# Kernel optimization log

Hardware: AMD Instinct MI355X
Metric: run time of the kernel (lower is better)

## Reference

```python
import jax, jax.numpy as jnp
import numpy as np

N_NODES = 50000
N_EDGES = 800000
F_IN = 128
HID = 32
H_IN = 4
N_CLS = 47
H_OUT = 4
NEG_SLOPE = 0.2


def _param(k, shape, scale=0.1):
    return jax.random.normal(k, shape, dtype=jnp.float32) * scale


def setup_inputs() -> dict:
    key = jax.random.key(0)
    ks = jax.random.split(key, 14)
    return {
        "x": jax.random.normal(ks[0], (N_NODES, F_IN), dtype=jnp.float32),
        "edge_index": jax.random.randint(ks[1], (2, N_EDGES), 0, N_NODES, dtype=jnp.int64),
        # layer 1: in -> hidden, heads_in, concat
        "W1": _param(ks[2], (F_IN, H_IN * HID)),
        "a1s": _param(ks[3], (H_IN, HID)),
        "a1d": _param(ks[4], (H_IN, HID)),
        "b1": _param(ks[5], (H_IN * HID,)),
        # layer 2: hidden*heads -> hidden, heads_in, concat
        "W2": _param(ks[6], (H_IN * HID, H_IN * HID)),
        "a2s": _param(ks[7], (H_IN, HID)),
        "a2d": _param(ks[8], (H_IN, HID)),
        "b2": _param(ks[9], (H_IN * HID,)),
        # layer 3: hidden*heads -> out, heads_out, mean (concat=False)
        "W3": _param(ks[10], (H_IN * HID, H_OUT * N_CLS)),
        "a3s": _param(ks[11], (H_OUT, N_CLS)),
        "a3d": _param(ks[12], (H_OUT, N_CLS)),
        "b3": _param(ks[13], (N_CLS,)),
    }


def gat_conv(x, W, att_src, att_dst, bias, src, dst, concat):
    """PyG GATConv (self-loops pre-appended in src/dst, eval mode)."""
    n = x.shape[0]
    H, C = att_src.shape
    h = (x @ W).reshape(n, H, C)                      # [N, H, C]
    a_src = jnp.sum(h * att_src[None], axis=-1)       # [N, H]
    a_dst = jnp.sum(h * att_dst[None], axis=-1)       # [N, H]
    alpha = a_src[src] + a_dst[dst]                   # [E, H]
    alpha = jnp.where(alpha >= 0, alpha, NEG_SLOPE * alpha)
    # segment softmax over destination nodes
    m = jax.ops.segment_max(alpha, dst, num_segments=n)  # [N, H]
    e = jnp.exp(alpha - m[dst])
    denom = jax.ops.segment_sum(e, dst, num_segments=n)  # [N, H]
    w = e / denom[dst]                                   # [E, H]
    msg = h[src] * w[:, :, None]                         # [E, H, C]
    out = jax.ops.segment_sum(msg, dst, num_segments=n)  # [N, H, C]
    if concat:
        out = out.reshape(n, H * C)
    else:
        out = out.mean(axis=1)
    return out + bias


def reference(x, edge_index, W1, a1s, a1d, b1, W2, a2s, a2d, b2, W3, a3s, a3d, b3):
    n = x.shape[0]
    loops = jnp.arange(n, dtype=edge_index.dtype)
    src = jnp.concatenate([edge_index[0], loops])
    dst = jnp.concatenate([edge_index[1], loops])
    h = gat_conv(x, W1, a1s, a1d, b1, src, dst, concat=True)
    h = jax.nn.relu(h)
    h = gat_conv(h, W2, a2s, a2d, b2, src, dst, concat=True)
    h = jax.nn.relu(h)
    h = gat_conv(h, W3, a3s, a3d, b3, src, dst, concat=False)
    return jax.nn.log_softmax(h, axis=1)
```

## Files before the change

### kernel.cpp

```cpp
#include <hip/hip_runtime.h>

typedef unsigned short u16;
typedef unsigned int uint32;
typedef __attribute__((ext_vector_type(8))) short short8;
typedef __attribute__((ext_vector_type(4))) float float4v;

#define N_NODES 50000
#define N_EDGES 800000
#define N_TOT   850000
#define NBH 256
#define NB_BKT ((N_NODES + 255) >> 8)
#define NODE_BLOCKS ((N_NODES + 3) / 4)

__device__ __forceinline__ float b2f(u16 u) {
  return __uint_as_float(((unsigned int)u) << 16);
}
__device__ __forceinline__ u16 f2b(float f) {
  unsigned int x = __float_as_uint(f);
  unsigned int r = (x + 0x7fffu + ((x >> 16) & 1u)) >> 16;
  return (u16)r;
}
__device__ __forceinline__ float lo_bf(uint32 g) { return __uint_as_float(g << 16); }
__device__ __forceinline__ float hi_bf(uint32 g) { return __uint_as_float(g & 0xffff0000u); }
__device__ __forceinline__ u16 conv_elem(const void* src, int i, int isf32) {
  if (isf32) return f2b(((const float*)src)[i]);
  return ((const u16*)src)[i];
}
__device__ __forceinline__ float lrelu(float a) { return (a >= 0.f) ? a : 0.2f * a; }
__device__ __forceinline__ int eget(const int* __restrict__ ei, int i, int isI64) {
  return isI64 ? ei[2 * i] : ei[i];
}

__global__ void detect_mode(const u16* __restrict__ x16, const int* __restrict__ ei32,
                            int* __restrict__ flags) {
  __shared__ int sh_f32, sh_i32;
  int tid = threadIdx.x;
  if (tid == 0) { sh_f32 = 0; sh_i32 = 0; }
  __syncthreads();
  int emax = 0;
  for (int i = tid; i < 4096; i += 256) {
    int e = (x16[i] >> 7) & 0xFF;
    emax = emax > e ? emax : e;
  }
  if (emax >= 140) atomicOr(&sh_f32, 1);
  if (ei32[2 * tid + 1] != 0) atomicOr(&sh_i32, 1);
  __syncthreads();
  if (tid == 0) { flags[0] = sh_f32; flags[1] = sh_i32 ? 0 : 1; }
}

__global__ void reorder_all(const void* W1, const void* W2, const void* W3,
                            const void* a1s, const void* a1d, const void* b1,
                            const void* a2s, const void* a2d, const void* b2,
                            const void* a3s, const void* a3d, const void* b3,
                            const int* __restrict__ flags,
                            u16* __restrict__ Wf1, u16* __restrict__ Wf2,
                            u16* __restrict__ Wf3, u16* __restrict__ wt) {
  int idx = blockIdx.x * blockDim.x + threadIdx.x;
  int f32 = flags[0];
  if (idx < 57344) {
    const void* W; u16* Wf; int NCOLS, li;
    if (idx < 16384)      { W = W1; Wf = Wf1; NCOLS = 128; li = idx; }
    else if (idx < 32768) { W = W2; Wf = Wf2; NCOLS = 128; li = idx - 16384; }
    else                  { W = W3; Wf = Wf3; NCOLS = 188; li = idx - 32768; }
    int j = li & 7;
    int l = (li >> 3) & 63;
    int c = (li >> 9) & 3;
    int t = li >> 11;
    int k = c * 32 + (l >> 4) * 8 + j;
    int n = t * 16 + (l & 15);
    Wf[li] = (n < NCOLS) ? conv_elem(W, k * NCOLS + n, f32) : (u16)0;
  } else {
    int li = idx - 57344;
    const void* src; int off;
    if (li < 128)       { src = a1s; off = 16384; }
    else if (li < 256)  { src = a1d; off = 16512; li -= 128; }
    else if (li < 384)  { src = b1;  off = 16640; li -= 256; }
    else if (li < 512)  { src = a2s; off = 33152; li -= 384; }
    else if (li < 640)  { src = a2d; off = 33280; li -= 512; }
    else if (li < 768)  { src = b2;  off = 33408; li -= 640; }
    else if (li < 956)  { src = a3s; off = 57600; li -= 768; }
    else if (li < 1144) { src = a3d; off = 57788; li -= 956; }
    else if (li < 1191) { src = b3;  off = 57976; li -= 1144; }
    else return;
    wt[off + li] = conv_elem(src, li, f32);
  }
}


__global__ __launch_bounds__(256) void pack_hist(const int* __restrict__ ei,
                                                 const int* __restrict__ flags,
                                                 uint32* __restrict__ epack,
                                                 int* __restrict__ cnt, int nE) {
  __shared__ int hist[NB_BKT];
  for (int t = threadIdx.x; t < NB_BKT; t += 256) hist[t] = 0;
  __syncthreads();
  const int i64 = flags[1];
  const int chunk = (nE + NBH - 1) / NBH;
  const int lo = blockIdx.x * chunk;
  const int hi = min(lo + chunk, nE);
  for (int e = lo + (int)threadIdx.x; e < hi; e += 256) {
    int s = eget(ei, e, i64);
    int d = eget(ei, nE + e, i64);
    epack[e] = ((uint32)d << 16) | (uint32)s;
    atomicAdd(&hist[d >> 8], 1);
  }
  __syncthreads();
  for (int t = threadIdx.x; t < NB_BKT; t += 256) cnt[t * NBH + blockIdx.x] = hist[t];
}

__global__ __launch_bounds__(256) void scan_cols(int* __restrict__ cnt,
                                                 int* __restrict__ total) {
  __shared__ int ws[4];
  const int bkt = blockIdx.x;
  const int tid = threadIdx.x, lane = tid & 63, wv = tid >> 6;
  int v = cnt[bkt * NBH + tid];
  int incl = v;
#pragma unroll
  for (int off = 1; off < 64; off <<= 1) {
    int t = __shfl_up(incl, off, 64);
    if (lane >= off) incl += t;
  }
  if (lane == 63) ws[wv] = incl;
  __syncthreads();
  if (tid == 0) {
    int s = 0;
#pragma unroll
    for (int w = 0; w < 4; w++) { int t = ws[w]; ws[w] = s; s += t; }
    total[bkt] = s;
  }
  __syncthreads();
  cnt[bkt * NBH + tid] = ws[wv] + incl - v;
}

__global__ __launch_bounds__(256) void scan_base(const int* __restrict__ total,
                                                 int* __restrict__ base) {
  __shared__ int ws[4];
  const int tid = threadIdx.x, lane = tid & 63, wv = tid >> 6;
  int v = (tid < NB_BKT) ? total[tid] : 0;
  int incl = v;
#pragma unroll
  for (int off = 1; off < 64; off <<= 1) {
    int t = __shfl_up(incl, off, 64);
    if (lane >= off) incl += t;
  }
  if (lane == 63) ws[wv] = incl;
  __syncthreads();
  if (tid == 0) {
    int s = 0;
#pragma unroll
    for (int w = 0; w < 4; w++) { int t = ws[w]; ws[w] = s; s += t; }
    base[NB_BKT] = s;
  }
  __syncthreads();
  if (tid < NB_BKT) base[tid] = ws[wv] + incl - v;
}

__global__ __launch_bounds__(256) void scatter_coarse(const uint32* __restrict__ epack,
                                                      const int* __restrict__ cnt,
                                                      const int* __restrict__ base,
                                                      uint32* __restrict__ staging, int nE) {
  __shared__ int lcur[NB_BKT];
  for (int t = threadIdx.x; t < NB_BKT; t += 256)
    lcur[t] = base[t] + cnt[t * NBH + blockIdx.x];
  __syncthreads();
  const int chunk = (nE + NBH - 1) / NBH;
  const int lo = blockIdx.x * chunk;
  const int hi = min(lo + chunk, nE);
  for (int e = lo + (int)threadIdx.x; e < hi; e += 256) {
    uint32 pk = epack[e];
    int p = atomicAdd(&lcur[pk >> 24], 1);
    staging[p] = pk;
  }
}

__global__ __launch_bounds__(256) void build_csr(const uint32* __restrict__ staging,
                                                 const int* __restrict__ base,
                                                 int* __restrict__ row_start,
                                                 u16* __restrict__ csr_dst,
                                                 int* __restrict__ csr_src32, int nN) {
  __shared__ int hist[256];
  __shared__ int cur[256];
  __shared__ int ws[4];
  const int b = blockIdx.x;
  const int tid = threadIdx.x;
  const int lane = tid & 63, wv = tid >> 6;
  hist[tid] = 0;
  __syncthreads();
  const int lo = base[b], hi = base[b + 1];
  for (int i = lo + tid; i < hi; i += 256)
    atomicAdd(&hist[(staging[i] >> 16) & 255], 1);
  __syncthreads();
  int v = hist[tid];
  int incl = v;
#pragma unroll
  for (int off = 1; off < 64; off <<= 1) {
    int t = __shfl_up(incl, off, 64);
    if (lane >= off) incl += t;
  }
  if (lane == 63) ws[wv] = incl;
  __syncthreads();
  if (tid == 0) {
    int s = 0;
#pragma unroll
    for (int w = 0; w < 4; w++) { int t = ws[w]; ws[w] = s; s += t; }
  }
  __syncthreads();
  int excl = ws[wv] + incl - v;
  const int n = (b << 8) + tid;
  if (n < nN) {
    int rs = lo + (b << 8) + excl + tid;
    row_start[n] = rs;
    csr_src32[rs] = n;
    u16 g16 = (u16)n;
    for (int k = 0; k <= v; k++) csr_dst[rs + k] = g16;
    cur[tid] = rs + 1;
  }
  if (b == NB_BKT - 1 && tid == 0) row_start[nN] = N_TOT;
  __syncthreads();
  for (int i = lo + tid; i < hi; i += 256) {
    uint32 pk = staging[i];
    int p = atomicAdd(&cur[(pk >> 16) & 255], 1);
    csr_src32[p] = (int)(pk & 0xffffu);
  }
}

template <int NT, int NCOLS, int STRIDE, bool FUSE_A, bool CMAJOR, bool FUSE3, bool RAWX>
__global__ __launch_bounds__(256) void gemm_mfma(const void* __restrict__ X,
                                                 const u16* __restrict__ Wf,
                                                 const u16* __restrict__ attS,
                                                 const u16* __restrict__ attD,
                                                 const int* __restrict__ flags,
                                                 u16* __restrict__ H,
                                                 float* __restrict__ a_s,
                                                 float* __restrict__ a_d, int M) {
  const int wid = __builtin_amdgcn_readfirstlane(threadIdx.x >> 6);
  const int lane = threadIdx.x & 63;
  const int row0 = (blockIdx.x * 4 + wid) * 16;
  if (row0 >= M) return;
  const int qr = lane >> 4;
  const int ln = lane & 15;

  float4v acc[NT];
#pragma unroll
  for (int t = 0; t < NT; t++) acc[t] = (float4v){0.f, 0.f, 0.f, 0.f};

  const short8* Wf8 = (const short8*)Wf;
  const size_t aoff = (size_t)(row0 + ln) * 128 + qr * 8;
  int f32m = 0;
  if constexpr (RAWX) f32m = flags[0];

#pragma unroll
  for (int c = 0; c < 4; c++) {
    short8 afrag;
    if constexpr (RAWX) {
      if (f32m) {
        const float* ap = (const float*)X + aoff + c * 32;
        float4 lo = ((const float4*)ap)[0];
        float4 hi = ((const float4*)ap)[1];
        afrag[0] = (short)f2b(lo.x); afrag[1] = (short)f2b(lo.y);
        afrag[2] = (short)f2b(lo.z); afrag[3] = (short)f2b(lo.w);
        afrag[4] = (short)f2b(hi.x); afrag[5] = (short)f2b(hi.y);
        afrag[6] = (short)f2b(hi.z); afrag[7] = (short)f2b(hi.w);
      } else {
        afrag = *(const short8*)((const u16*)X + aoff + c * 32);
      }
    } else {
      afrag = *(const short8*)((const u16*)X + aoff + c * 32);
    }
#pragma unroll
    for (int t = 0; t < NT; t++) {
      short8 bfrag = Wf8[(t * 4 + c) * 64 + lane];
      acc[t] = __builtin_amdgcn_mfma_f32_16x16x32_bf16(afrag, bfrag, acc[t], 0, 0, 0);
    }
  }

#pragma unroll
  for (int t = 0; t < NT; t++) {
    int col = t * 16 + ln;
    if (col < NCOLS) {
      int off;
      if constexpr (CMAJOR) {
        int h = (col >= 141) ? 3 : (col >= 94) ? 2 : (col >= 47) ? 1 : 0;
        int c = col - h * 47;
        off = c * 4 + h;
      } else {
        off = col;
      }
#pragma unroll
      for (int i = 0; i < 4; i++) {
        H[(size_t)(row0 + qr * 4 + i) * STRIDE + off] = f2b(acc[t][i]);
      }
    } else {
      if constexpr (CMAJOR) {
#pragma unroll
        for (int i = 0; i < 4; i++) {
          H[(size_t)(row0 + qr * 4 + i) * STRIDE + col] = (u16)0x3F80;
        }
      }
    }
  }

  if constexpr (FUSE_A) {
    float aSf[NT], aDf[NT];
#pragma unroll
    for (int t = 0; t < NT; t++) {
      aSf[t] = b2f(attS[t * 16 + ln]);
      aDf[t] = b2f(attD[t * 16 + ln]);
    }
#pragma unroll
    for (int h = 0; h < 4; h++) {
#pragma unroll
      for (int i = 0; i < 4; i++) {
        float s = acc[2 * h][i] * aSf[2 * h] + acc[2 * h + 1][i] * aSf[2 * h + 1];
        float d = acc[2 * h][i] * aDf[2 * h] + acc[2 * h + 1][i] * aDf[2 * h + 1];
#pragma unroll
        for (int m = 1; m < 16; m <<= 1) {
          s += __shfl_xor(s, m, 64);
          d += __shfl_xor(d, m, 64);
        }
        if (ln == 0) {
          int r = row0 + qr * 4 + i;
          a_s[r * 4 + h] = s;
          a_d[r * 4 + h] = d;
        }
      }
    }
  }

  if constexpr (FUSE3) {
    float sh[4][4], dh[4][4];
#pragma unroll
    for (int h = 0; h < 4; h++)
#pragma unroll
      for (int i = 0; i < 4; i++) { sh[h][i] = 0.f; dh[h][i] = 0.f; }
#pragma unroll
    for (int t = 0; t < NT; t++) {
      int col = t * 16 + ln;
      bool v = (col < NCOLS);
      float aS = v ? b2f(attS[col]) : 0.f;
      float aD = v ? b2f(attD[col]) : 0.f;
      int hh = (col >= 141) ? 3 : (col >= 94) ? 2 : (col >= 47) ? 1 : 0;
      float aS0 = (hh == 0) ? aS : 0.f, aS1 = (hh == 1) ? aS : 0.f;
      float aS2 = (hh == 2) ? aS : 0.f, aS3 = (hh == 3) ? aS : 0.f;
      float aD0 = (hh == 0) ? aD : 0.f, aD1 = (hh == 1) ? aD : 0.f;
      float aD2 = (hh == 2) ? aD : 0.f, aD3 = (hh == 3) ? aD : 0.f;
#pragma unroll
      for (int i = 0; i < 4; i++) {
        float a = acc[t][i];
        sh[0][i] += a * aS0; sh[1][i] += a * aS1;
        sh[2][i] += a * aS2; sh[3][i] += a * aS3;
        dh[0][i] += a * aD0; dh[1][i] += a * aD1;
        dh[2][i] += a * aD2; dh[3][i] += a * aD3;
      }
    }
#pragma unroll
    for (int h = 0; h < 4; h++) {
#pragma unroll
      for (int i = 0; i < 4; i++) {
        float s = sh[h][i], d = dh[h][i];
#pragma unroll
        for (int m = 1; m < 16; m <<= 1) {
          s += __shfl_xor(s, m, 64);
          d += __shfl_xor(d, m, 64);
        }
        if (ln == 0) {
          int r = row0 + qr * 4 + i;
          a_s[r * 4 + h] = s;
          a_d[r * 4 + h] = d;
        }
      }
    }
  }
}

__global__ __launch_bounds__(256) void edge_weights(const int* __restrict__ csr_src,
                                                    const u16* __restrict__ csr_dst,
                                                    const float* __restrict__ a_s,
                                                    const float* __restrict__ a_d,
                                                    uint2* __restrict__ w, int nE) {
  int e = blockIdx.x * blockDim.x + threadIdx.x;
  if (e >= nE) return;
  int s = csr_src[e], d = csr_dst[e];
  float4 as = ((const float4*)a_s)[s];
  float4 ad = ((const float4*)a_d)[d];
  float w0 = __expf(lrelu(as.x + ad.x));
  float w1 = __expf(lrelu(as.y + ad.y));
  float w2 = __expf(lrelu(as.z + ad.z));
  float w3 = __expf(lrelu(as.w + ad.w));
  uint2 o;
  o.x = ((uint32)f2b(w1) << 16) | (uint32)f2b(w0);
  o.y = ((uint32)f2b(w3) << 16) | (uint32)f2b(w2);
  w[e] = o;
}


__global__ __launch_bounds__(256) void aggregate12(const u16* __restrict__ h,
                                                   const float* __restrict__ a_s,
                                                   const float* __restrict__ a_d,
                                                   const int* __restrict__ row_start,
                                                   const int* __restrict__ csr_src,
                                                   const u16* __restrict__ bias,
                                                   u16* __restrict__ out, int nN) {
  const int lane = threadIdx.x & 63;
  const int wid = __builtin_amdgcn_readfirstlane(threadIdx.x >> 6);
  const int n = blockIdx.x * 4 + wid;
  if (n >= nN) return;
  const int hL = lane >> 4;
  const uint32* h32 = (const uint32*)h;
  const float bias0 = b2f(bias[2 * lane]);
  const float bias1 = b2f(bias[2 * lane + 1]);
  const float adv = a_d[n * 4 + hL];
  int beg = row_start[n], end = row_start[n + 1];

  float acc0 = 0.f, acc1 = 0.f, den = 0.f;
  int e = beg;
  for (; e + 3 < end; e += 4) {
    int s[4];
    float av[4];
    uint32 g[4];
#pragma unroll
    for (int j = 0; j < 4; j++) s[j] = csr_src[e + j];
#pragma unroll
    for (int j = 0; j < 4; j++) av[j] = a_s[s[j] * 4 + hL];
#pragma unroll
    for (int j = 0; j < 4; j++) g[j] = h32[s[j] * 64 + lane];
#pragma unroll
    for (int j = 0; j < 4; j++) {
      float w = __expf(lrelu(av[j] + adv));
      den += w;
      acc0 += w * lo_bf(g[j]);
      acc1 += w * hi_bf(g[j]);
    }
  }
  for (; e < end; ++e) {
    int s = csr_src[e];
    float w = __expf(lrelu(a_s[s * 4 + hL] + adv));
    uint32 g = h32[s * 64 + lane];
    den += w;
    acc0 += w * lo_bf(g);
    acc1 += w * hi_bf(g);
  }
  float inv = 1.0f / den;
  float o0 = fmaxf(acc0 * inv + bias0, 0.f);
  float o1 = fmaxf(acc1 * inv + bias1, 0.f);
  uint32 packed = ((uint32)f2b(o1) << 16) | (uint32)f2b(o0);
  ((uint32*)out)[n * 64 + lane] = packed;
}

__global__ __launch_bounds__(256) void aggregate3(const u16* __restrict__ h3,
                                                  const uint2* __restrict__ wbuf,
                                                  const int* __restrict__ row_start,
                                                  const int* __restrict__ csr_src,
                                                  const u16* __restrict__ b3,
                                                  const int* __restrict__ flags,
                                                  void* __restrict__ out, int nN) {
  const int lane = threadIdx.x & 63;
  const int wid = __builtin_amdgcn_readfirstlane(threadIdx.x >> 6);
  const int n = blockIdx.x * 4 + wid;
  if (n >= nN) return;
  const bool act = lane < 47;
  const int lidx = (lane <= 47) ? lane : 0;
  const float b3v = act ? b2f(b3[lane]) : 0.f;
  const int isf32 = flags[0];
  const uint2* h3v = (const uint2*)h3;
  int beg = row_start[n], end = row_start[n + 1];

  float acc0 = 0.f, acc1 = 0.f, acc2 = 0.f, acc3 = 0.f;
  int e = beg;
  for (; e + 7 < end; e += 8) {
    int s[8];
    uint2 wp[8];
    uint2 g[8];
#pragma unroll
    for (int j = 0; j < 8; j++) s[j] = csr_src[e + j];
#pragma unroll
    for (int j = 0; j < 8; j++) wp[j] = wbuf[e + j];
#pragma unroll
    for (int j = 0; j < 8; j++) g[j] = h3v[(size_t)s[j] * 48 + lidx];
#pragma unroll
    for (int j = 0; j < 8; j++) {
      float w0 = lo_bf(wp[j].x), w1 = hi_bf(wp[j].x);
      float w2 = lo_bf(wp[j].y), w3 = hi_bf(wp[j].y);
      acc0 += w0 * lo_bf(g[j].x);
      acc1 += w1 * hi_bf(g[j].x);
      acc2 += w2 * lo_bf(g[j].y);
      acc3 += w3 * hi_bf(g[j].y);
    }
  }
  for (; e + 3 < end; e += 4) {
    int s[4];
    uint2 wp[4];
    uint2 g[4];
#pragma unroll
    for (int j = 0; j < 4; j++) s[j] = csr_src[e + j];
#pragma unroll
    for (int j = 0; j < 4; j++) wp[j] = wbuf[e + j];
#pragma unroll
    for (int j = 0; j < 4; j++) g[j] = h3v[(size_t)s[j] * 48 + lidx];
#pragma unroll
    for (int j = 0; j < 4; j++) {
      float w0 = lo_bf(wp[j].x), w1 = hi_bf(wp[j].x);
      float w2 = lo_bf(wp[j].y), w3 = hi_bf(wp[j].y);
      acc0 += w0 * lo_bf(g[j].x);
      acc1 += w1 * hi_bf(g[j].x);
      acc2 += w2 * lo_bf(g[j].y);
      acc3 += w3 * hi_bf(g[j].y);
    }
  }
  for (; e < end; ++e) {
    int s = csr_src[e];
    uint2 wp = wbuf[e];
    uint2 g = h3v[(size_t)s * 48 + lidx];
    float w0 = lo_bf(wp.x), w1 = hi_bf(wp.x);
    float w2 = lo_bf(wp.y), w3 = hi_bf(wp.y);
    acc0 += w0 * lo_bf(g.x);
    acc1 += w1 * hi_bf(g.x);
    acc2 += w2 * lo_bf(g.y);
    acc3 += w3 * hi_bf(g.y);
  }
  float den0 = __shfl(acc0, 47, 64);
  float den1 = __shfl(acc1, 47, 64);
  float den2 = __shfl(acc2, 47, 64);
  float den3 = __shfl(acc3, 47, 64);
  float val = act ? 0.25f * (acc0 / den0 + acc1 / den1 + acc2 / den2 + acc3 / den3) + b3v
                  : -1e30f;
  float mx = val;
#pragma unroll
  for (int m = 1; m < 64; m <<= 1) mx = fmaxf(mx, __shfl_xor(mx, m, 64));
  float ex = act ? __expf(val - mx) : 0.f;
  float sm = ex;
#pragma unroll
  for (int m = 1; m < 64; m <<= 1) sm += __shfl_xor(sm, m, 64);
  float lse = mx + __logf(sm);
  if (act) {
    float r = val - lse;
    if (isf32) ((float*)out)[n * 47 + lane] = r;
    else       ((u16*)out)[n * 47 + lane] = f2b(r);
  }
}


extern "C" void kernel_launch(void* const* d_in, const int* in_sizes, int n_in,
                              void* d_out, int out_size, void* d_ws, size_t ws_size,
                              hipStream_t stream) {
  const void* x   = d_in[0];
  const void* ei  = d_in[1];
  const void* W1  = d_in[2];
  const void* a1s = d_in[3];
  const void* a1d = d_in[4];
  const void* b1  = d_in[5];
  const void* W2  = d_in[6];
  const void* a2s = d_in[7];
  const void* a2d = d_in[8];
  const void* b2  = d_in[9];
  const void* W3  = d_in[10];
  const void* a3s = d_in[11];
  const void* a3d = d_in[12];
  const void* b3  = d_in[13];
  const int* ei32 = (const int*)ei;

  auto au = [](size_t v) { return (v + 255) & ~(size_t)255; };
  char* p = (char*)d_ws;
  int* flags     = (int*)p; p += 256;
  u16* wt        = (u16*)p; p += au((size_t)58023 * 2);
  u16* Wf1       = (u16*)p; p += au((size_t)16384 * 2);
  u16* Wf2       = (u16*)p; p += au((size_t)16384 * 2);
  u16* Wf3       = (u16*)p; p += au((size_t)24576 * 2);
  int* row_start = (int*)p; p += au((size_t)(N_NODES + 1) * 4);
  int* cnt       = (int*)p; p += au((size_t)NB_BKT * NBH * 4);
  int* btotal    = (int*)p; p += au((size_t)NB_BKT * 4);
  int* bbase     = (int*)p; p += au((size_t)(NB_BKT + 1) * 4);
  int* csr_src32 = (int*)p; p += au((size_t)N_TOT * 4);
  u16* csr_dst   = (u16*)p; p += au((size_t)N_TOT * 2);
  uint2* wbuf    = (uint2*)p; p += au((size_t)N_TOT * 8);
  float* a_s     = (float*)p; p += au((size_t)N_NODES * 4 * 4);
  float* a_d     = (float*)p; p += au((size_t)N_NODES * 4 * 4);
  u16* hB        = (u16*)p; p += au((size_t)N_NODES * 128 * 2);
  u16* hA        = (u16*)p; p += au((size_t)N_NODES * 128 * 2);
  u16* h3        = (u16*)p; p += au((size_t)N_NODES * 192 * 2);
  uint32* epack   = (uint32*)h3;
  uint32* staging = (uint32*)(h3 + 1600000);

  const u16* a1sc = wt + 16384;
  const u16* a1dc = wt + 16512;
  const u16* b1c  = wt + 16640;
  const u16* a2sc = wt + 33152;
  const u16* a2dc = wt + 33280;
  const u16* b2c  = wt + 33408;
  const u16* a3sc = wt + 57600;
  const u16* a3dc = wt + 57788;
  const u16* b3c  = wt + 57976;

  const int gemmBlocks = (N_NODES / 16 + 3) / 4;
  const int edgeBlocks = (N_TOT + 255) / 256;

  detect_mode<<<1, 256, 0, stream>>>((const u16*)x, ei32, flags);
  reorder_all<<<229, 256, 0, stream>>>(W1, W2, W3, a1s, a1d, b1, a2s, a2d, b2,
                                       a3s, a3d, b3, flags, Wf1, Wf2, Wf3, wt);

  pack_hist<<<NBH, 256, 0, stream>>>(ei32, flags, epack, cnt, N_EDGES);
  scan_cols<<<NB_BKT, 256, 0, stream>>>(cnt, btotal);
  scan_base<<<1, 256, 0, stream>>>(btotal, bbase);
  scatter_coarse<<<NBH, 256, 0, stream>>>(epack, cnt, bbase, staging, N_EDGES);
  build_csr<<<NB_BKT, 256, 0, stream>>>(staging, bbase, row_start, csr_dst,
                                        csr_src32, N_NODES);

  gemm_mfma<8, 128, 128, true, false, false, true><<<gemmBlocks, 256, 0, stream>>>(
      x, Wf1, a1sc, a1dc, flags, hA, a_s, a_d, N_NODES);
  aggregate12<<<NODE_BLOCKS, 256, 0, stream>>>(hA, a_s, a_d, row_start, csr_src32,
                                               b1c, hB, N_NODES);

  gemm_mfma<8, 128, 128, true, false, false, false><<<gemmBlocks, 256, 0, stream>>>(
      hB, Wf2, a2sc, a2dc, flags, hA, a_s, a_d, N_NODES);
  aggregate12<<<NODE_BLOCKS, 256, 0, stream>>>(hA, a_s, a_d, row_start, csr_src32,
                                               b2c, hB, N_NODES);

  gemm_mfma<12, 188, 192, false, true, true, false><<<gemmBlocks, 256, 0, stream>>>(
      hB, Wf3, a3sc, a3dc, flags, h3, a_s, a_d, N_NODES);
  edge_weights<<<edgeBlocks, 256, 0, stream>>>(csr_src32, csr_dst, a_s, a_d, wbuf, N_TOT);
  aggregate3<<<NODE_BLOCKS, 256, 0, stream>>>(h3, wbuf, row_start, csr_src32,
                                              b3c, flags, d_out, N_NODES);
}
```

Baseline: 311.7 us.

## Fuse graph preprocessing kernels into one persistent kernel with grid barriers

Replaces seven small preprocessing launches (mode detection, weight reorder, histogram, two scans, scatter, CSR build) with a single 256-block kernel that separates the phases with atomic-counter grid barriers, reset by a memset. The goal is to remove per-launch overhead and idle gaps between tiny kernels. It depends on all 256 blocks being resident at once, and every block now repeats the mode-detection reads. Separately, the layer 1/2 aggregation loop gets an 8-edge unrolled path to put more gathers in flight.

```diff
diff --git a/kernel.cpp b/kernel.cpp
--- a/kernel.cpp
+++ b/kernel.cpp
@@ -31,196 +31,195 @@
   return isI64 ? ei[2 * i] : ei[i];
 }
 
-__global__ void detect_mode(const u16* __restrict__ x16, const int* __restrict__ ei32,
-                            int* __restrict__ flags) {
-  __shared__ int sh_f32, sh_i32;
-  int tid = threadIdx.x;
-  if (tid == 0) { sh_f32 = 0; sh_i32 = 0; }
+__device__ __forceinline__ void gbar(int* bar, int target) {
   __syncthreads();
-  int emax = 0;
-  for (int i = tid; i < 4096; i += 256) {
-    int e = (x16[i] >> 7) & 0xFF;
-    emax = emax > e ? emax : e;
-  }
-  if (emax >= 140) atomicOr(&sh_f32, 1);
-  if (ei32[2 * tid + 1] != 0) atomicOr(&sh_i32, 1);
+  if (threadIdx.x == 0) {
+    __threadfence();
+    atomicAdd(bar, 1);
+    while (atomicAdd(bar, 0) < target) __builtin_amdgcn_s_sleep(8);
+    __threadfence();
+  }
   __syncthreads();
-  if (tid == 0) { flags[0] = sh_f32; flags[1] = sh_i32 ? 0 : 1; }
-}
-
-__global__ void reorder_all(const void* W1, const void* W2, const void* W3,
-                            const void* a1s, const void* a1d, const void* b1,
-                            const void* a2s, const void* a2d, const void* b2,
-                            const void* a3s, const void* a3d, const void* b3,
-                            const int* __restrict__ flags,
-                            u16* __restrict__ Wf1, u16* __restrict__ Wf2,
-                            u16* __restrict__ Wf3, u16* __restrict__ wt) {
-  int idx = blockIdx.x * blockDim.x + threadIdx.x;
-  int f32 = flags[0];
-  if (idx < 57344) {
-    const void* W; u16* Wf; int NCOLS, li;
-    if (idx < 16384)      { W = W1; Wf = Wf1; NCOLS = 128; li = idx; }
-    else if (idx < 32768) { W = W2; Wf = Wf2; NCOLS = 128; li = idx - 16384; }
-    else                  { W = W3; Wf = Wf3; NCOLS = 188; li = idx - 32768; }
-    int j = li & 7;
-    int l = (li >> 3) & 63;
-    int c = (li >> 9) & 3;
-    int t = li >> 11;
-    int k = c * 32 + (l >> 4) * 8 + j;
-    int n = t * 16 + (l & 15);
-    Wf[li] = (n < NCOLS) ? conv_elem(W, k * NCOLS + n, f32) : (u16)0;
-  } else {
-    int li = idx - 57344;
-    const void* src; int off;
-    if (li < 128)       { src = a1s; off = 16384; }
-    else if (li < 256)  { src = a1d; off = 16512; li -= 128; }
-    else if (li < 384)  { src = b1;  off = 16640; li -= 256; }
-    else if (li < 512)  { src = a2s; off = 33152; li -= 384; }
-    else if (li < 640)  { src = a2d; off = 33280; li -= 512; }
-    else if (li < 768)  { src = b2;  off = 33408; li -= 640; }
-    else if (li < 956)  { src = a3s; off = 57600; li -= 768; }
-    else if (li < 1144) { src = a3d; off = 57788; li -= 956; }
-    else if (li < 1191) { src = b3;  off = 57976; li -= 1144; }
-    else return;
-    wt[off + li] = conv_elem(src, li, f32);
-  }
-}
-
-
-__global__ __launch_bounds__(256) void pack_hist(const int* __restrict__ ei,
-                                                 const int* __restrict__ flags,
-                                                 uint32* __restrict__ epack,
-                                                 int* __restrict__ cnt, int nE) {
-  __shared__ int hist[NB_BKT];
-  for (int t = threadIdx.x; t < NB_BKT; t += 256) hist[t] = 0;
-  __syncthreads();
-  const int i64 = flags[1];
-  const int chunk = (nE + NBH - 1) / NBH;
-  const int lo = blockIdx.x * chunk;
-  const int hi = min(lo + chunk, nE);
-  for (int e = lo + (int)threadIdx.x; e < hi; e += 256) {
-    int s = eget(ei, e, i64);
-    int d = eget(ei, nE + e, i64);
-    epack[e] = ((uint32)d << 16) | (uint32)s;
-    atomicAdd(&hist[d >> 8], 1);
-  }
-  __syncthreads();
-  for (int t = threadIdx.x; t < NB_BKT; t += 256) cnt[t * NBH + blockIdx.x] = hist[t];
-}
-
-__global__ __launch_bounds__(256) void scan_cols(int* __restrict__ cnt,
-                                                 int* __restrict__ total) {
-  __shared__ int ws[4];
-  const int bkt = blockIdx.x;
-  const int tid = threadIdx.x, lane = tid & 63, wv = tid >> 6;
-  int v = cnt[bkt * NBH + tid];
-  int incl = v;
-#pragma unroll
-  for (int off = 1; off < 64; off <<= 1) {
-    int t = __shfl_up(incl, off, 64);
-    if (lane >= off) incl += t;
-  }
-  if (lane == 63) ws[wv] = incl;
-  __syncthreads();
-  if (tid == 0) {
-    int s = 0;
-#pragma unroll
-    for (int w = 0; w < 4; w++) { int t = ws[w]; ws[w] = s; s += t; }
-    total[bkt] = s;
-  }
-  __syncthreads();
-  cnt[bkt * NBH + tid] = ws[wv] + incl - v;
-}
-
-__global__ __launch_bounds__(256) void scan_base(const int* __restrict__ total,
-                                                 int* __restrict__ base) {
-  __shared__ int ws[4];
-  const int tid = threadIdx.x, lane = tid & 63, wv = tid >> 6;
-  int v = (tid < NB_BKT) ? total[tid] : 0;
-  int incl = v;
-#pragma unroll
-  for (int off = 1; off < 64; off <<= 1) {
-    int t = __shfl_up(incl, off, 64);
-    if (lane >= off) incl += t;
-  }
-  if (lane == 63) ws[wv] = incl;
-  __syncthreads();
-  if (tid == 0) {
-    int s = 0;
-#pragma unroll
-    for (int w = 0; w < 4; w++) { int t = ws[w]; ws[w] = s; s += t; }
-    base[NB_BKT] = s;
-  }
-  __syncthreads();
-  if (tid < NB_BKT) base[tid] = ws[wv] + incl - v;
-}
-
-__global__ __launch_bounds__(256) void scatter_coarse(const uint32* __restrict__ epack,
-                                                      const int* __restrict__ cnt,
-                                                      const int* __restrict__ base,
-                                                      uint32* __restrict__ staging, int nE) {
-  __shared__ int lcur[NB_BKT];
-  for (int t = threadIdx.x; t < NB_BKT; t += 256)
-    lcur[t] = base[t] + cnt[t * NBH + blockIdx.x];
-  __syncthreads();
-  const int chunk = (nE + NBH - 1) / NBH;
-  const int lo = blockIdx.x * chunk;
-  const int hi = min(lo + chunk, nE);
-  for (int e = lo + (int)threadIdx.x; e < hi; e += 256) {
-    uint32 pk = epack[e];
-    int p = atomicAdd(&lcur[pk >> 24], 1);
-    staging[p] = pk;
-  }
-}
-
-__global__ __launch_bounds__(256) void build_csr(const uint32* __restrict__ staging,
-                                                 const int* __restrict__ base,
-                                                 int* __restrict__ row_start,
-                                                 u16* __restrict__ csr_dst,
-                                                 int* __restrict__ csr_src32, int nN) {
-  __shared__ int hist[256];
-  __shared__ int cur[256];
-  __shared__ int ws[4];
-  const int b = blockIdx.x;
+}
+
+__global__ __launch_bounds__(256) void mega_front(
+    const u16* __restrict__ x16, const int* __restrict__ ei32,
+    const void* W1, const void* W2, const void* W3,
+    const void* a1s, const void* a1d, const void* b1,
+    const void* a2s, const void* a2d, const void* b2,
+    const void* a3s, const void* a3d, const void* b3,
+    int* __restrict__ flags,
+    u16* __restrict__ Wf1, u16* __restrict__ Wf2, u16* __restrict__ Wf3,
+    u16* __restrict__ wt,
+    int* __restrict__ cnt, int* __restrict__ btotal, int* __restrict__ bbase,
+    uint32* __restrict__ epack, uint32* __restrict__ staging,
+    int* __restrict__ row_start, u16* __restrict__ csr_dst,
+    int* __restrict__ csr_src32, int* __restrict__ bar) {
+  __shared__ int shA[256];
+  __shared__ int shB[256];
+  __shared__ int shW[4];
+  __shared__ int shF[2];
   const int tid = threadIdx.x;
   const int lane = tid & 63, wv = tid >> 6;
-  hist[tid] = 0;
+
+  if (tid == 0) { shF[0] = 0; shF[1] = 0; }
   __syncthreads();
-  const int lo = base[b], hi = base[b + 1];
-  for (int i = lo + tid; i < hi; i += 256)
-    atomicAdd(&hist[(staging[i] >> 16) & 255], 1);
+  {
+    int emax = 0;
+    for (int i = tid; i < 4096; i += 256) {
+      int e = (x16[i] >> 7) & 0xFF;
+      emax = emax > e ? emax : e;
+    }
+    if (emax >= 140) atomicOr(&shF[0], 1);
+    if (ei32[2 * tid + 1] != 0) atomicOr(&shF[1], 1);
+  }
   __syncthreads();
-  int v = hist[tid];
-  int incl = v;
-#pragma unroll
-  for (int off = 1; off < 64; off <<= 1) {
-    int t = __shfl_up(incl, off, 64);
-    if (lane >= off) incl += t;
-  }
-  if (lane == 63) ws[wv] = incl;
+  const int f32 = shF[0];
+  const int i64 = shF[1] ? 0 : 1;
+  if (blockIdx.x == 0 && tid == 0) { flags[0] = f32; flags[1] = i64; }
+
+  {
+    int idx = blockIdx.x * 256 + tid;
+    if (idx < 57344) {
+      const void* W; u16* Wf; int NCOLS, li;
+      if (idx < 16384)      { W = W1; Wf = Wf1; NCOLS = 128; li = idx; }
+      else if (idx < 32768) { W = W2; Wf = Wf2; NCOLS = 128; li = idx - 16384; }
+      else                  { W = W3; Wf = Wf3; NCOLS = 188; li = idx - 32768; }
+      int j = li & 7;
+      int l = (li >> 3) & 63;
+      int c = (li >> 9) & 3;
+      int t = li >> 11;
+      int k = c * 32 + (l >> 4) * 8 + j;
+      int n = t * 16 + (l & 15);
+      Wf[li] = (n < NCOLS) ? conv_elem(W, k * NCOLS + n, f32) : (u16)0;
+    } else if (idx < 58535) {
+      int li = idx - 57344;
+      const void* src; int off;
+      if (li < 128)       { src = a1s; off = 16384; }
+      else if (li < 256)  { src = a1d; off = 16512; li -= 128; }
+      else if (li < 384)  { src = b1;  off = 16640; li -= 256; }
+      else if (li < 512)  { src = a2s; off = 33152; li -= 384; }
+      else if (li < 640)  { src = a2d; off = 33280; li -= 512; }
+      else if (li < 768)  { src = b2;  off = 33408; li -= 640; }
+      else if (li < 956)  { src = a3s; off = 57600; li -= 768; }
+      else if (li < 1144) { src = a3d; off = 57788; li -= 956; }
+      else                { src = b3;  off = 57976; li -= 1144; }
+      wt[off + li] = conv_elem(src, li, f32);
+    }
+  }
+
+  for (int t = tid; t < NB_BKT; t += 256) shA[t] = 0;
   __syncthreads();
-  if (tid == 0) {
-    int s = 0;
-#pragma unroll
-    for (int w = 0; w < 4; w++) { int t = ws[w]; ws[w] = s; s += t; }
+  const int chunk = (N_EDGES + NBH - 1) / NBH;
+  const int elo = blockIdx.x * chunk;
+  const int ehi = min(elo + chunk, N_EDGES);
+  for (int e = elo + tid; e < ehi; e += 256) {
+    int s = eget(ei32, e, i64);
+    int d = eget(ei32, N_EDGES + e, i64);
+    epack[e] = ((uint32)d << 16) | (uint32)s;
+    atomicAdd(&shA[d >> 8], 1);
   }
   __syncthreads();
-  int excl = ws[wv] + incl - v;
-  const int n = (b << 8) + tid;
-  if (n < nN) {
-    int rs = lo + (b << 8) + excl + tid;
-    row_start[n] = rs;
-    csr_src32[rs] = n;
-    u16 g16 = (u16)n;
-    for (int k = 0; k <= v; k++) csr_dst[rs + k] = g16;
-    cur[tid] = rs + 1;
-  }
-  if (b == NB_BKT - 1 && tid == 0) row_start[nN] = N_TOT;
+  for (int t = tid; t < NB_BKT; t += 256) cnt[t * NBH + blockIdx.x] = shA[t];
+
+  gbar(bar, NBH);
+
+  if (blockIdx.x < NB_BKT) {
+    const int bkt = blockIdx.x;
+    int v = cnt[bkt * NBH + tid];
+    int incl = v;
+#pragma unroll
+    for (int off = 1; off < 64; off <<= 1) {
+      int t = __shfl_up(incl, off, 64);
+      if (lane >= off) incl += t;
+    }
+    if (lane == 63) shW[wv] = incl;
+    __syncthreads();
+    if (tid == 0) {
+      int s = 0;
+#pragma unroll
+      for (int w = 0; w < 4; w++) { int t = shW[w]; shW[w] = s; s += t; }
+      btotal[bkt] = s;
+    }
+    __syncthreads();
+    cnt[bkt * NBH + tid] = shW[wv] + incl - v;
+  }
+
+  gbar(bar, 2 * NBH);
+
+  if (blockIdx.x == 0) {
+    int v = (tid < NB_BKT) ? btotal[tid] : 0;
+    int incl = v;
+#pragma unroll
+    for (int off = 1; off < 64; off <<= 1) {
+      int t = __shfl_up(incl, off, 64);
+      if (lane >= off) incl += t;
+    }
+    if (lane == 63) shW[wv] = incl;
+    __syncthreads();
+    if (tid == 0) {
+      int s = 0;
+#pragma unroll
+      for (int w = 0; w < 4; w++) { int t = shW[w]; shW[w] = s; s += t; }
+      bbase[NB_BKT] = s;
+    }
+    __syncthreads();
+    if (tid < NB_BKT) bbase[tid] = shW[wv] + incl - v;
+  }
+
+  gbar(bar, 3 * NBH);
+
+  for (int t = tid; t < NB_BKT; t += 256)
+    shA[t] = bbase[t] + cnt[t * NBH + blockIdx.x];
   __syncthreads();
-  for (int i = lo + tid; i < hi; i += 256) {
-    uint32 pk = staging[i];
-    int p = atomicAdd(&cur[(pk >> 16) & 255], 1);
-    csr_src32[p] = (int)(pk & 0xffffu);
+  for (int e = elo + tid; e < ehi; e += 256) {
+    uint32 pk = epack[e];
+    int p = atomicAdd(&shA[pk >> 24], 1);
+    staging[p] = pk;
+  }
+
+  gbar(bar, 4 * NBH);
+
+  if (blockIdx.x < NB_BKT) {
+    const int b = blockIdx.x;
+    shA[tid] = 0;
+    __syncthreads();
+    const int lo = bbase[b], hi = bbase[b + 1];
+    for (int i = lo + tid; i < hi; i += 256)
+      atomicAdd(&shA[(staging[i] >> 16) & 255], 1);
+    __syncthreads();
+    int v = shA[tid];
+    int incl = v;
+#pragma unroll
+    for (int off = 1; off < 64; off <<= 1) {
+      int t = __shfl_up(incl, off, 64);
+      if (lane >= off) incl += t;
+    }
+    if (lane == 63) shW[wv] = incl;
+    __syncthreads();
+    if (tid == 0) {
+      int s = 0;
+#pragma unroll
+      for (int w = 0; w < 4; w++) { int t = shW[w]; shW[w] = s; s += t; }
+    }
+    __syncthreads();
+    int excl = shW[wv] + incl - v;
+    const int n = (b << 8) + tid;
+    if (n < N_NODES) {
+      int rs = lo + (b << 8) + excl + tid;
+      row_start[n] = rs;
+      csr_src32[rs] = n;
+      u16 g16 = (u16)n;
+      for (int k = 0; k <= v; k++) csr_dst[rs + k] = g16;
+      shB[tid] = rs + 1;
+    }
+    if (b == NB_BKT - 1 && tid == 0) row_start[N_NODES] = N_TOT;
+    __syncthreads();
+    for (int i = lo + tid; i < hi; i += 256) {
+      uint32 pk = staging[i];
+      int p = atomicAdd(&shB[(pk >> 16) & 255], 1);
+      csr_src32[p] = (int)(pk & 0xffffu);
+    }
   }
 }
 
@@ -414,6 +413,24 @@
 
   float acc0 = 0.f, acc1 = 0.f, den = 0.f;
   int e = beg;
+  for (; e + 7 < end; e += 8) {
+    int s[8];
+    float av[8];
+    uint32 g[8];
+#pragma unroll
+    for (int j = 0; j < 8; j++) s[j] = csr_src[e + j];
+#pragma unroll
+    for (int j = 0; j < 8; j++) av[j] = a_s[s[j] * 4 + hL];
+#pragma unroll
+    for (int j = 0; j < 8; j++) g[j] = h32[s[j] * 64 + lane];
+#pragma unroll
+    for (int j = 0; j < 8; j++) {
+      float w = __expf(lrelu(av[j] + adv));
+      den += w;
+      acc0 += w * lo_bf(g[j]);
+      acc1 += w * hi_bf(g[j]);
+    }
+  }
   for (; e + 3 < end; e += 4) {
     int s[4];
     float av[4];
@@ -562,6 +579,7 @@
   auto au = [](size_t v) { return (v + 255) & ~(size_t)255; };
   char* p = (char*)d_ws;
   int* flags     = (int*)p; p += 256;
+  int* bar       = (int*)p; p += 256;
   u16* wt        = (u16*)p; p += au((size_t)58023 * 2);
   u16* Wf1       = (u16*)p; p += au((size_t)16384 * 2);
   u16* Wf2       = (u16*)p; p += au((size_t)16384 * 2);
@@ -594,16 +612,13 @@
   const int gemmBlocks = (N_NODES / 16 + 3) / 4;
   const int edgeBlocks = (N_TOT + 255) / 256;
 
-  detect_mode<<<1, 256, 0, stream>>>((const u16*)x, ei32, flags);
-  reorder_all<<<229, 256, 0, stream>>>(W1, W2, W3, a1s, a1d, b1, a2s, a2d, b2,
-                                       a3s, a3d, b3, flags, Wf1, Wf2, Wf3, wt);
-
-  pack_hist<<<NBH, 256, 0, stream>>>(ei32, flags, epack, cnt, N_EDGES);
-  scan_cols<<<NB_BKT, 256, 0, stream>>>(cnt, btotal);
-  scan_base<<<1, 256, 0, stream>>>(btotal, bbase);
-  scatter_coarse<<<NBH, 256, 0, stream>>>(epack, cnt, bbase, staging, N_EDGES);
-  build_csr<<<NB_BKT, 256, 0, stream>>>(staging, bbase, row_start, csr_dst,
-                                        csr_src32, N_NODES);
+  hipMemsetAsync(bar, 0, 4, stream);
+
+  mega_front<<<NBH, 256, 0, stream>>>((const u16*)x, ei32, W1, W2, W3,
+                                      a1s, a1d, b1, a2s, a2d, b2, a3s, a3d, b3,
+                                      flags, Wf1, Wf2, Wf3, wt,
+                                      cnt, btotal, bbase, epack, staging,
+                                      row_start, csr_dst, csr_src32, bar);
 
   gemm_mfma<8, 128, 128, true, false, false, true><<<gemmBlocks, 256, 0, stream>>>(
       x, Wf1, a1sc, a1dc, flags, hA, a_s, a_d, N_NODES);
```

Measured after the change: 384.7 us. 23.4% more time.
